# Performance work log

Measured on AMD Instinct MI355X. Metric: run time of the kernel, lower is better.

The kernel has to match this reference:

```python
import jax, jax.numpy as jnp
import numpy as np

B, T = 32, 512
DA, DV = 1280, 768
D = DA + DV          # fused audio+video feature dim = 2048
DM = 256             # mamba d_model
L = 4                # n_layers
DI = 2 * DM          # d_inner (expand=2)
DS = 16              # d_state
DC = 4               # d_conv
R = DM // 16         # dt_rank = ceil(256/16)
H = 128              # attn-pool hidden
NC = 8               # emotion classes
EPS_TIN = 1e-5
EPS_LN = 1e-5


def _ln(x, g, b):
    mu = x.mean(-1, keepdims=True)
    v = ((x - mu) ** 2).mean(-1, keepdims=True)
    return (x - mu) / jnp.sqrt(v + EPS_LN) * g + b


def _mamba(u, in_w, cw, cb, xw, dtw, dtb, A_log, Dp, ow):
    # u: [B,T,DM] -> [B,T,DM]; Mamba(v1) selective scan, d_state=16, d_conv=4, expand=2
    xz = jnp.einsum('btd,ed->bte', u, in_w)            # [B,T,2*DI]
    x, z = xz[..., :DI], xz[..., DI:]
    xp = jnp.pad(x, ((0, 0), (DC - 1, 0), (0, 0)))     # causal depthwise conv1d
    xc = sum(xp[:, k:k + u.shape[1], :] * cw[:, k] for k in range(DC)) + cb
    x = jax.nn.silu(xc)
    dbc = jnp.einsum('btd,ed->bte', x, xw)             # [B,T,R+2*DS]
    dt = jax.nn.softplus(jnp.einsum('btr,dr->btd', dbc[..., :R], dtw) + dtb)
    Bm = dbc[..., R:R + DS]
    Cm = dbc[..., R + DS:]
    A = -jnp.exp(A_log)                                # [DI,DS]

    def step(h, inp):
        dt_t, B_t, C_t, x_t = inp                      # [B,DI],[B,DS],[B,DS],[B,DI]
        h = jnp.exp(dt_t[..., None] * A) * h + dt_t[..., None] * B_t[:, None, :] * x_t[..., None]
        return h, jnp.einsum('bds,bs->bd', h, C_t)

    h0 = jnp.zeros((u.shape[0], DI, DS), u.dtype)
    xs = (dt.swapaxes(0, 1), Bm.swapaxes(0, 1), Cm.swapaxes(0, 1), x.swapaxes(0, 1))
    _, ys = jax.lax.scan(step, h0, xs)
    y = ys.swapaxes(0, 1) + Dp * x
    y = y * jax.nn.silu(z)
    return jnp.einsum('bti,oi->bto', y, ow)


def _forward(x, tin_gamma, tin_beta, proj_w, proj_b, ln_g, ln_b, in_proj_w, conv_w, conv_b,
             x_proj_w, dt_proj_w, dt_proj_b, A_log, D_param, out_proj_w,
             out_ln_g, out_ln_b, res_scale, attn_w1, attn_b1, attn_w2, head_w, head_b, lengths):
    mask = jnp.arange(T)[None, :] < lengths[:, None]   # [B,T]
    m = mask[..., None].astype(x.dtype)
    # FusedTIN: masked temporal instance norm + affine
    denom = jnp.maximum(lengths, 1).astype(x.dtype)[:, None, None]
    mean = (x * m).sum(1, keepdims=True) / denom
    var = (((x - mean) ** 2) * m).sum(1, keepdims=True) / denom
    xn = (x - mean) / jnp.sqrt(var + EPS_TIN) * m
    xn = (xn * tin_gamma + tin_beta) * m
    # MambaStack: proj_in + prenorm residual mamba blocks (dropout = eval identity)
    h = jnp.einsum('btd,md->btm', xn, proj_w) + proj_b
    for l in range(L):
        y = _mamba(_ln(h, ln_g[l], ln_b[l]), in_proj_w[l], conv_w[l], conv_b[l],
                   x_proj_w[l], dt_proj_w[l], dt_proj_b[l], A_log[l], D_param[l], out_proj_w[l])
        h = h + res_scale * y
    h = _ln(h, out_ln_g, out_ln_b)
    # MaskedAttnPool
    s = jnp.einsum('bth,oh->bto', jnp.tanh(jnp.einsum('btd,hd->bth', h, attn_w1) + attn_b1), attn_w2)[..., 0]
    logits = jnp.where(mask, s, -jnp.inf)
    alpha = jnp.nan_to_num(jax.nn.softmax(logits, axis=1)) * mask
    alpha = alpha / jnp.clip(alpha.sum(1, keepdims=True), 1e-9)
    ctx = (alpha[..., None] * h).sum(1)
    # classifier head
    return jnp.einsum('bd,cd->bc', ctx, head_w) + head_b


def setup_inputs() -> dict:
    key = jax.random.key(0)
    ks = jax.random.split(key, 16)
    s = 0.05
    inp = {}
    inp['x'] = jax.random.normal(ks[0], (B, T, D), jnp.float32)
    inp['lengths'] = jax.random.randint(ks[1], (B,), T // 4, T + 1)
    inp['tin_gamma'] = jnp.ones((D,), jnp.float32)
    inp['tin_beta'] = jnp.zeros((D,), jnp.float32)
    inp['proj_w'] = jax.random.normal(ks[2], (DM, D), jnp.float32) * s
    inp['proj_b'] = jnp.zeros((DM,), jnp.float32)
    inp['ln_g'] = jnp.ones((L, DM), jnp.float32)
    inp['ln_b'] = jnp.zeros((L, DM), jnp.float32)
    inp['in_proj_w'] = jax.random.normal(ks[3], (L, 2 * DI, DM), jnp.float32) * s
    inp['conv_w'] = jax.random.normal(ks[4], (L, DI, DC), jnp.float32) * s
    inp['conv_b'] = jnp.zeros((L, DI), jnp.float32)
    inp['x_proj_w'] = jax.random.normal(ks[5], (L, R + 2 * DS, DI), jnp.float32) * s
    inp['dt_proj_w'] = jax.random.normal(ks[6], (L, DI, R), jnp.float32) * s
    inp['dt_proj_b'] = jnp.full((L, DI), -3.0, jnp.float32) + jax.random.normal(ks[7], (L, DI), jnp.float32) * 0.1
    inp['A_log'] = jnp.log(jnp.broadcast_to(jnp.arange(1, DS + 1, dtype=jnp.float32), (L, DI, DS)) + 0.0)
    inp['D_param'] = jnp.ones((L, DI), jnp.float32)
    inp['out_proj_w'] = jax.random.normal(ks[8], (L, DM, DI), jnp.float32) * s
    inp['out_ln_g'] = jnp.ones((DM,), jnp.float32)
    inp['out_ln_b'] = jnp.zeros((DM,), jnp.float32)
    inp['res_scale'] = jnp.asarray(0.1, jnp.float32)
    inp['attn_w1'] = jax.random.normal(ks[9], (H, DM), jnp.float32) * s
    inp['attn_b1'] = jnp.zeros((H,), jnp.float32)
    inp['attn_w2'] = jax.random.normal(ks[10], (1, H), jnp.float32) * s
    inp['head_w'] = jax.random.normal(ks[11], (NC, DM), jnp.float32) * s
    inp['head_b'] = jnp.zeros((NC,), jnp.float32)
    return inp


def reference(x, tin_gamma, tin_beta, proj_w, proj_b, ln_g, ln_b, in_proj_w, conv_w, conv_b,
              x_proj_w, dt_proj_w, dt_proj_b, A_log, D_param, out_proj_w,
              out_ln_g, out_ln_b, res_scale, attn_w1, attn_b1, attn_w2, head_w, head_b, lengths):
    return _forward(x, tin_gamma, tin_beta, proj_w, proj_b, ln_g, ln_b, in_proj_w, conv_w, conv_b,
                    x_proj_w, dt_proj_w, dt_proj_b, A_log, D_param, out_proj_w,
                    out_ln_g, out_ln_b, res_scale, attn_w1, attn_b1, attn_w2, head_w, head_b, lengths)
```

## Files before the change

### kernel.cpp

```cpp
#include <hip/hip_runtime.h>

#define NB 32
#define NT 512
#define ND 2048
#define NDM 256
#define NDI 512
#define NDS 16
#define NR 16
#define NH 128
#define NNC 8
#define NL 4
#define NM (NB*NT)

typedef __attribute__((ext_vector_type(8))) short short8;
typedef __attribute__((ext_vector_type(4))) float floatx4;

__device__ __forceinline__ unsigned short f2bf_rn(float f) {
    unsigned u = __builtin_bit_cast(unsigned, f);
    u += 0x7FFFu + ((u >> 16) & 1u);
    return (unsigned short)(u >> 16);
}
__device__ __forceinline__ void cvt8(const float* v, short8& h8, short8& l8) {
#pragma unroll
    for (int q = 0; q < 8; ++q) {
        unsigned short hb = f2bf_rn(v[q]);
        float hf = __builtin_bit_cast(float, (unsigned)hb << 16);
        h8[q] = (short)hb;
        l8[q] = (short)f2bf_rn(v[q] - hf);
    }
}
__device__ __forceinline__ float quad_sum(float v) {
    int i = __builtin_bit_cast(int, v);
    int j = __builtin_amdgcn_update_dpp(0, i, 0xB1, 0xF, 0xF, true);
    v += __builtin_bit_cast(float, j);
    i = __builtin_bit_cast(int, v);
    j = __builtin_amdgcn_update_dpp(0, i, 0x4E, 0xF, 0xF, true);
    v += __builtin_bit_cast(float, j);
    return v;
}
__device__ __forceinline__ void glds16(const short* g, short* lds_base) {
    __builtin_amdgcn_global_load_lds(
        (const __attribute__((address_space(1))) void*)g,
        (__attribute__((address_space(3))) void*)lds_base, 16, 0, 0);
}

__global__ __launch_bounds__(256) void tin_stats_k(
    const float* __restrict__ x, const int* __restrict__ lengths,
    float* __restrict__ mean, float* __restrict__ rstd)
{
    __shared__ float rs_[4][64];
    __shared__ float rq_[4][64];
    const int b = blockIdx.x >> 5;
    const int d0 = (blockIdx.x & 31) << 6;
    const int dl = threadIdx.x & 63;
    const int strip = threadIdx.x >> 6;
    const int len = lengths[b];
    const int d = d0 + dl;
    float s = 0.f, q = 0.f;
    for (int t = strip; t < len; t += 4) {
        float v = x[((size_t)(b*NT + t))*ND + d];
        s += v; q += v*v;
    }
    rs_[strip][dl] = s; rq_[strip][dl] = q;
    __syncthreads();
    if (threadIdx.x < 64) {
        float S = rs_[0][dl]+rs_[1][dl]+rs_[2][dl]+rs_[3][dl];
        float Q = rq_[0][dl]+rq_[1][dl]+rq_[2][dl]+rq_[3][dl];
        float inv = 1.f / (float)(len < 1 ? 1 : len);
        float mu = S * inv;
        float var = Q * inv - mu*mu;
        mean[b*ND + d] = mu;
        rstd[b*ND + d] = rsqrtf(var + 1e-5f);
    }
}

#define SLN 264
__global__ __launch_bounds__(256) void tin_norm_k(
    const float* __restrict__ x, const int* __restrict__ lengths,
    const float* __restrict__ mean, const float* __restrict__ rstd,
    const float* __restrict__ g, const float* __restrict__ be,
    short* __restrict__ Oh, short* __restrict__ Ol)
{
    __shared__ float sT[16][SLN];
    const int tid = threadIdx.x;
    const int row = tid >> 4, c = tid & 15;
    const int m = blockIdx.x*16 + row;
    const int b = m >> 9, t = m & (NT-1);
    const int len = lengths[b];
    const int kg0 = blockIdx.y*256 + c*16;
    if (t >= len) {
#pragma unroll
        for (int i = 0; i < 16; ++i) sT[row][c*16 + i] = 0.f;
    } else {
#pragma unroll
        for (int qq = 0; qq < 4; ++qq) {
            const int kg = kg0 + qq*4;
            float4 v = *(const float4*)(x + (size_t)m*ND + kg);
            float4 mn = *(const float4*)(mean + b*ND + kg);
            float4 rr = *(const float4*)(rstd + b*ND + kg);
            float4 gg = *(const float4*)(g + kg);
            float4 bb = *(const float4*)(be + kg);
            sT[row][c*16+qq*4+0] = (v.x-mn.x)*rr.x*gg.x + bb.x;
            sT[row][c*16+qq*4+1] = (v.y-mn.y)*rr.y*gg.y + bb.y;
            sT[row][c*16+qq*4+2] = (v.z-mn.z)*rr.z*gg.z + bb.z;
            sT[row][c*16+qq*4+3] = (v.w-mn.w)*rr.w*gg.w + bb.w;
        }
    }
    __syncthreads();
#pragma unroll
    for (int q = 0; q < 2; ++q) {
        const int slot = tid + 256*q;
        const int tile = slot >> 6, ln2 = slot & 63;
        const int mr = ln2 & 15, kc = ln2 >> 4;
        float v[8];
        *(float4*)&v[0] = *(const float4*)&sT[mr][tile*32 + kc*8];
        *(float4*)&v[4] = *(const float4*)&sT[mr][tile*32 + kc*8 + 4];
        short8 h8, l8; cvt8(v, h8, l8);
        const size_t off = ((size_t)blockIdx.x*64 + blockIdx.y*8 + tile)*512 + ln2*8;
        *(short8*)(Oh + off) = h8;
        *(short8*)(Ol + off) = l8;
    }
}

__global__ __launch_bounds__(256) void wconv_k(
    const float* __restrict__ W, short* __restrict__ Oh, short* __restrict__ Ol,
    int K, int nmod, int nvalid)
{
    __shared__ float sT[16][SLN];
    const int tid = threadIdx.x;
    const int row = tid >> 4, c = tid & 15;
    const int n = blockIdx.x*16 + row;
    const int rr = n % nmod;
    const int kg0 = blockIdx.y*256 + c*16;
    if (rr >= nvalid) {
#pragma unroll
        for (int i = 0; i < 16; ++i) sT[row][c*16 + i] = 0.f;
    } else {
        const int src = (n/nmod)*nvalid + rr;
#pragma unroll
        for (int qq = 0; qq < 4; ++qq) {
            float4 v = *(const float4*)(W + (size_t)src*K + kg0 + qq*4);
            *(float4*)&sT[row][c*16+qq*4] = v;
        }
    }
    __syncthreads();
#pragma unroll
    for (int q = 0; q < 2; ++q) {
        const int slot = tid + 256*q;
        const int tile = slot >> 6, ln2 = slot & 63;
        const int mr = ln2 & 15, kc = ln2 >> 4;
        float v[8];
        *(float4*)&v[0] = *(const float4*)&sT[mr][tile*32 + kc*8];
        *(float4*)&v[4] = *(const float4*)&sT[mr][tile*32 + kc*8 + 4];
        short8 h8, l8; cvt8(v, h8, l8);
        const size_t off = ((size_t)blockIdx.x*(K>>5) + blockIdx.y*8 + tile)*512 + ln2*8;
        *(short8*)(Oh + off) = h8;
        *(short8*)(Ol + off) = l8;
    }
}

template<int MSUB, int NSUB, int EPI, int ATOMIC>
__global__ __launch_bounds__(256) void mgemm_k(
    const short* __restrict__ Ah, const short* __restrict__ Al,
    const short* __restrict__ Bh, const short* __restrict__ Bl,
    const float* __restrict__ bias, float* __restrict__ C,
    int ldc, int Nvalid, int K, const float* __restrict__ rsp)
{
    __shared__ __align__(16) short lds[(MSUB+NSUB)*1024];
    short* As_h = lds;
    short* As_l = lds + MSUB*512;
    short* Bs_h = lds + MSUB*1024;
    short* Bs_l = lds + MSUB*1024 + NSUB*512;
    const int tid = threadIdx.x, lane = tid & 63, w = tid >> 6;
    const int m0t = blockIdx.x * MSUB;
    const int n0t = blockIdx.y * NSUB;
    const int Ktiles = K >> 5;
    const int kslice = Ktiles / (int)gridDim.z;
    const int kt0 = blockIdx.z * kslice;
    constexpr int MI = MSUB/2, NI = NSUB/2;
    constexpr int ASG = MSUB/4, BSG = NSUB/4;
    const int wm = w >> 1, wn = w & 1;

    floatx4 acc[MI][NI] = {};

    for (int kk = 0; kk < kslice; ++kk) {
        const int kb = kt0 + kk;
#pragma unroll
        for (int u = 0; u < ASG; ++u) {
            const int sub = w*ASG + u;
            const size_t off = ((size_t)(m0t + sub)*Ktiles + kb)*512 + lane*8;
            glds16(Ah + off, &As_h[sub*512]);
            glds16(Al + off, &As_l[sub*512]);
        }
#pragma unroll
        for (int u = 0; u < BSG; ++u) {
            const int sub = w*BSG + u;
            const size_t off = ((size_t)(n0t + sub)*Ktiles + kb)*512 + lane*8;
            glds16(Bh + off, &Bs_h[sub*512]);
            glds16(Bl + off, &Bs_l[sub*512]);
        }
        __syncthreads();
        short8 fah[MI], fal[MI], fbh[NI], fbl[NI];
#pragma unroll
        for (int i = 0; i < MI; ++i) {
            const int sub = wm*MI + i;
            fah[i] = *(const short8*)&As_h[sub*512 + lane*8];
            fal[i] = *(const short8*)&As_l[sub*512 + lane*8];
        }
#pragma unroll
        for (int j = 0; j < NI; ++j) {
            const int sub = wn*NI + j;
            fbh[j] = *(const short8*)&Bs_h[sub*512 + lane*8];
            fbl[j] = *(const short8*)&Bs_l[sub*512 + lane*8];
        }
#pragma unroll
        for (int i = 0; i < MI; ++i)
#pragma unroll
            for (int j = 0; j < NI; ++j) {
                acc[i][j] = __builtin_amdgcn_mfma_f32_16x16x32_bf16(fah[i], fbh[j], acc[i][j], 0, 0, 0);
                acc[i][j] = __builtin_amdgcn_mfma_f32_16x16x32_bf16(fah[i], fbl[j], acc[i][j], 0, 0, 0);
                acc[i][j] = __builtin_amdgcn_mfma_f32_16x16x32_bf16(fal[i], fbh[j], acc[i][j], 0, 0, 0);
            }
        __syncthreads();
    }

    const float rs = (EPI == 1) ? rsp[0] : 0.f;
    const int lc = lane >> 4, col = lane & 15;
    const bool addb = (EPI != 1) && bias && (!ATOMIC || blockIdx.z == 0);
#pragma unroll
    for (int j = 0; j < NI; ++j) {
        const int n = (n0t + wn*NI + j)*16 + col;
        if (n < Nvalid) {
            const float bv = addb ? bias[n] : 0.f;
#pragma unroll
            for (int i = 0; i < MI; ++i) {
                const int mb = (m0t + wm*MI + i)*16 + lc*4;
#pragma unroll
                for (int r = 0; r < 4; ++r) {
                    float v = acc[i][j][r];
                    float* cp = C + (size_t)(mb + r)*ldc + n;
                    if (ATOMIC) {
                        if (EPI == 1) atomicAdd(cp, rs*v);
                        else          atomicAdd(cp, v + bv);
                    } else {
                        if (EPI == 0)      *cp = v + bv;
                        else if (EPI == 1) *cp = fmaf(rs, v, *cp);
                        else               *cp = tanhf(v + bv);
                    }
                }
            }
        }
    }
}

template<int WF32>
__global__ __launch_bounds__(256) void ln_blk_k(
    const float* __restrict__ in, const float* __restrict__ g,
    const float* __restrict__ b,
    short* __restrict__ Oh, short* __restrict__ Ol, float* __restrict__ o32)
{
    __shared__ float sT[16][SLN];
    const int tid = threadIdx.x;
    const int row = tid >> 4, c = tid & 15;
    const int m = blockIdx.x*16 + row;
    float v[16];
#pragma unroll
    for (int qq = 0; qq < 4; ++qq)
        *(float4*)&v[qq*4] = *(const float4*)(in + (size_t)m*NDM + c*16 + qq*4);
    float s = 0.f, q = 0.f;
#pragma unroll
    for (int i = 0; i < 16; ++i) { s += v[i]; q += v[i]*v[i]; }
#pragma unroll
    for (int o = 8; o; o >>= 1) { s += __shfl_xor(s, o); q += __shfl_xor(q, o); }
    const float mu = s * (1.f/NDM);
    const float r = rsqrtf(q*(1.f/NDM) - mu*mu + 1e-5f);
#pragma unroll
    for (int i = 0; i < 16; ++i) {
        const int kg = c*16 + i;
        v[i] = (v[i]-mu)*r*g[kg] + b[kg];
        sT[row][kg] = v[i];
    }
    if (WF32) {
#pragma unroll
        for (int qq = 0; qq < 4; ++qq)
            *(float4*)(o32 + (size_t)m*NDM + c*16 + qq*4) = *(const float4*)&v[qq*4];
    }
    __syncthreads();
#pragma unroll
    for (int qv = 0; qv < 2; ++qv) {
        const int slot = tid + 256*qv;
        const int tile = slot >> 6, ln2 = slot & 63;
        const int mr = ln2 & 15, kc = ln2 >> 4;
        float vv[8];
        *(float4*)&vv[0] = *(const float4*)&sT[mr][tile*32 + kc*8];
        *(float4*)&vv[4] = *(const float4*)&sT[mr][tile*32 + kc*8 + 4];
        short8 h8, l8; cvt8(vv, h8, l8);
        const size_t off = ((size_t)blockIdx.x*8 + tile)*512 + ln2*8;
        *(short8*)(Oh + off) = h8;
        *(short8*)(Ol + off) = l8;
    }
}

#define SCV 520
__global__ __launch_bounds__(256) void conv_blk_k(
    const float* __restrict__ xz, const float* __restrict__ cw,
    const float* __restrict__ cb, float* __restrict__ xc32,
    short* __restrict__ Oh, short* __restrict__ Ol)
{
    __shared__ float sT[16][SCV];
    const int tid = threadIdx.x;
    const int row = tid >> 4, cg = tid & 15;
    const int m = blockIdx.x*16 + row;
    const int t = m & (NT-1);
#pragma unroll
    for (int grp = 0; grp < 4; ++grp) {
        const int ch = cg*32 + grp*8;
        float a[8];
        *(float4*)&a[0] = *(const float4*)(cb + ch);
        *(float4*)&a[4] = *(const float4*)(cb + ch + 4);
        float4 wv[8];
#pragma unroll
        for (int i = 0; i < 8; ++i) wv[i] = *(const float4*)(cw + (ch+i)*4);
#pragma unroll
        for (int kk = 0; kk < 4; ++kk) {
            if (t - 3 + kk >= 0) {
                const float* xp = xz + (size_t)(m-3+kk)*(2*NDI) + ch;
                float xv[8];
                *(float4*)&xv[0] = *(const float4*)xp;
                *(float4*)&xv[4] = *(const float4*)(xp + 4);
                const float tap[8] = {
                    kk==0?wv[0].x:kk==1?wv[0].y:kk==2?wv[0].z:wv[0].w,
                    kk==0?wv[1].x:kk==1?wv[1].y:kk==2?wv[1].z:wv[1].w,
                    kk==0?wv[2].x:kk==1?wv[2].y:kk==2?wv[2].z:wv[2].w,
                    kk==0?wv[3].x:kk==1?wv[3].y:kk==2?wv[3].z:wv[3].w,
                    kk==0?wv[4].x:kk==1?wv[4].y:kk==2?wv[4].z:wv[4].w,
                    kk==0?wv[5].x:kk==1?wv[5].y:kk==2?wv[5].z:wv[5].w,
                    kk==0?wv[6].x:kk==1?wv[6].y:kk==2?wv[6].z:wv[6].w,
                    kk==0?wv[7].x:kk==1?wv[7].y:kk==2?wv[7].z:wv[7].w};
#pragma unroll
                for (int i = 0; i < 8; ++i) a[i] = fmaf(xv[i], tap[i], a[i]);
            }
        }
#pragma unroll
        for (int i = 0; i < 8; ++i) a[i] = a[i] / (1.f + __expf(-a[i]));
        *(float4*)&sT[row][ch] = *(const float4*)&a[0];
        *(float4*)&sT[row][ch+4] = *(const float4*)&a[4];
        *(float4*)(xc32 + (size_t)m*NDI + ch) = *(const float4*)&a[0];
        *(float4*)(xc32 + (size_t)m*NDI + ch + 4) = *(const float4*)&a[4];
    }
    __syncthreads();
#pragma unroll
    for (int q = 0; q < 4; ++q) {
        const int slot = tid + 256*q;
        const int tile = slot >> 6, ln2 = slot & 63;
        const int mr = ln2 & 15, kc = ln2 >> 4;
        float vv[8];
        *(float4*)&vv[0] = *(const float4*)&sT[mr][tile*32 + kc*8];
        *(float4*)&vv[4] = *(const float4*)&sT[mr][tile*32 + kc*8 + 4];
        short8 h8, l8; cvt8(vv, h8, l8);
        const size_t off = ((size_t)blockIdx.x*16 + tile)*512 + ln2*8;
        *(short8*)(Oh + off) = h8;
        *(short8*)(Ol + off) = l8;
    }
}

__global__ __launch_bounds__(256) void dt_k(
    const float* __restrict__ dbc, const float* __restrict__ dtw,
    const float* __restrict__ dtb, float* __restrict__ dt)
{
    const int m = blockIdx.x;
    const float* rsrc = dbc + (size_t)m*48;
    float rv[16];
#pragma unroll
    for (int i = 0; i < 16; ++i) rv[i] = rsrc[i];
#pragma unroll
    for (int hh = 0; hh < 2; ++hh) {
        const int d = hh*256 + threadIdx.x;
        const float* wr = dtw + d*16;
        float a = dtb[d];
#pragma unroll
        for (int i = 0; i < 16; ++i) a = fmaf(rv[i], wr[i], a);
        dt[(size_t)m*NDI + d] = (a > 20.f) ? a : log1pf(__expf(a));
    }
}

__global__ __launch_bounds__(256) void scan_k(
    const float* __restrict__ dbc, const float* __restrict__ dtp,
    const float* __restrict__ xcp, const float* __restrict__ xz,
    const float* __restrict__ Alog, const float* __restrict__ Dp,
    short* __restrict__ Yh, short* __restrict__ Yl)
{
    __shared__ float sBC[64][32];
    __shared__ float sDt[64][68];
    __shared__ float sX[64][68];
    __shared__ float sY[64][68];
    const int tid = threadIdx.x;
    const int w = tid >> 6, lane = tid & 63;
    const int dl = lane >> 2, sg = lane & 3;
    const int b = blockIdx.x >> 3;
    const int d0 = (blockIdx.x & 7) << 6;
    const int dloc = w*16 + dl;
    const int d = d0 + dloc;
    float ar[4];
    {
        float4 al4 = *(const float4*)(Alog + d*NDS + sg*4);
        ar[0] = -__expf(al4.x); ar[1] = -__expf(al4.y);
        ar[2] = -__expf(al4.z); ar[3] = -__expf(al4.w);
    }
    const float Dpv = Dp[d];
    float hr[4] = {0.f, 0.f, 0.f, 0.f};
    const int mbase = b*NT;
    const int srow = tid >> 2, sq = (tid & 3) << 3;
    const int tr = tid >> 2, qq = tid & 3;

    for (int c0 = 0; c0 < NT; c0 += 64) {
        __syncthreads();
        {
            const float* dp_ = dbc + (size_t)(mbase + c0 + srow)*48 + 16 + sq;
            *(float4*)&sBC[srow][sq]   = *(const float4*)dp_;
            *(float4*)&sBC[srow][sq+4] = *(const float4*)(dp_ + 4);
        }
        {
            const float* dsrc = dtp + (size_t)(mbase + c0 + tr)*NDI + d0 + qq*16;
            const float* xsrc = xcp + (size_t)(mbase + c0 + tr)*NDI + d0 + qq*16;
#pragma unroll
            for (int i = 0; i < 4; ++i) {
                float4 dv = *(const float4*)(dsrc + i*4);
                float4 xv = *(const float4*)(xsrc + i*4);
                const int dd = qq*16 + i*4;
                sDt[dd+0][tr]=dv.x; sDt[dd+1][tr]=dv.y; sDt[dd+2][tr]=dv.z; sDt[dd+3][tr]=dv.w;
                sX[dd+0][tr]=xv.x;  sX[dd+1][tr]=xv.y;  sX[dd+2][tr]=xv.z;  sX[dd+3][tr]=xv.w;
            }
        }
        __syncthreads();
        float4 Bt[2][4], Ct[2][4], dt4[2], x4[2];
#pragma unroll
        for (int i = 0; i < 4; ++i) {
            Bt[0][i] = *(const float4*)&sBC[i][sg*4];
            Ct[0][i] = *(const float4*)&sBC[i][16 + sg*4];
        }
        dt4[0] = *(const float4*)&sDt[dloc][0];
        x4[0]  = *(const float4*)&sX[dloc][0];
#pragma unroll
        for (int g = 0; g < 16; ++g) {
            const int cur = g & 1, nxt = cur ^ 1;
            if (g < 15) {
                const int t4 = (g+1)*4;
#pragma unroll
                for (int i = 0; i < 4; ++i) {
                    Bt[nxt][i] = *(const float4*)&sBC[t4+i][sg*4];
                    Ct[nxt][i] = *(const float4*)&sBC[t4+i][16 + sg*4];
                }
                dt4[nxt] = *(const float4*)&sDt[dloc][t4];
                x4[nxt]  = *(const float4*)&sX[dloc][t4];
            }
#pragma unroll
            for (int i = 0; i < 4; ++i) {
                const float dtv = (i==0)?dt4[cur].x:(i==1)?dt4[cur].y:(i==2)?dt4[cur].z:dt4[cur].w;
                const float xv  = (i==0)?x4[cur].x:(i==1)?x4[cur].y:(i==2)?x4[cur].z:x4[cur].w;
                const float4 Bv = Bt[cur][i];
                const float4 Cv = Ct[cur][i];
                const float dbx = dtv * xv;
                float pa0 = __expf(dtv*ar[0]);
                float pa1 = __expf(dtv*ar[1]);
                float pa2 = __expf(dtv*ar[2]);
                float pa3 = __expf(dtv*ar[3]);
                hr[0] = fmaf(pa0, hr[0], dbx*Bv.x);
                hr[1] = fmaf(pa1, hr[1], dbx*Bv.y);
                hr[2] = fmaf(pa2, hr[2], dbx*Bv.z);
                hr[3] = fmaf(pa3, hr[3], dbx*Bv.w);
                float cp = hr[0]*Cv.x;
                cp = fmaf(hr[1], Cv.y, cp);
                cp = fmaf(hr[2], Cv.z, cp);
                cp = fmaf(hr[3], Cv.w, cp);
                cp = quad_sum(cp);
                if (sg == 0) sY[g*4 + i][dloc] = fmaf(Dpv, xv, cp);
            }
        }
        __syncthreads();
#pragma unroll
        for (int q = 0; q < 2; ++q) {
            const int slot = tid + 256*q;
            const int tile = slot >> 6, ln2 = slot & 63;
            const int tm = tile >> 1, tk = tile & 1;
            const int mr = ln2 & 15, kc = ln2 >> 4;
            const int m = mbase + c0 + tm*16 + mr;
            const int kd = d0 + tk*32 + kc*8;
            float yv[8];
            *(float4*)&yv[0] = *(const float4*)&sY[tm*16 + mr][tk*32 + kc*8];
            *(float4*)&yv[4] = *(const float4*)&sY[tm*16 + mr][tk*32 + kc*8 + 4];
            float zv[8];
            *(float4*)&zv[0] = *(const float4*)(xz + (size_t)m*(2*NDI) + NDI + kd);
            *(float4*)&zv[4] = *(const float4*)(xz + (size_t)m*(2*NDI) + NDI + kd + 4);
#pragma unroll
            for (int i = 0; i < 8; ++i)
                yv[i] *= zv[i] / (1.f + __expf(-zv[i]));
            short8 h8, l8; cvt8(yv, h8, l8);
            const size_t off = ((size_t)(m>>4)*16 + (kd>>5))*512 + ln2*8;
            *(short8*)(Yh + off) = h8;
            *(short8*)(Yl + off) = l8;
        }
    }
}

__global__ __launch_bounds__(64) void score_k(
    const float* __restrict__ t1, const float* __restrict__ w2,
    float* __restrict__ sout)
{
    const int m = blockIdx.x;
    const int lane = threadIdx.x;
    float v = t1[(size_t)m*NH + lane]*w2[lane]
            + t1[(size_t)m*NH + 64 + lane]*w2[64 + lane];
#pragma unroll
    for (int o = 32; o; o >>= 1) v += __shfl_xor(v, o);
    if (lane == 0) sout[m] = v;
}

__global__ __launch_bounds__(256) void pool_k(
    const float* __restrict__ sbuf, const float* __restrict__ u,
    const int* __restrict__ lengths, float* __restrict__ ctx)
{
    __shared__ float al[NT];
    __shared__ float red[256];
    const int b = blockIdx.x;
    const int tid = threadIdx.x;
    const int len = lengths[b];
    float mx = -3.4e38f;
    for (int t = tid; t < len; t += 256) mx = fmaxf(mx, sbuf[b*NT + t]);
    red[tid] = mx; __syncthreads();
    for (int o = 128; o; o >>= 1) { if (tid < o) red[tid] = fmaxf(red[tid], red[tid+o]); __syncthreads(); }
    mx = red[0];
    __syncthreads();
    float sm = 0.f;
    for (int t = tid; t < len; t += 256) {
        float e = __expf(sbuf[b*NT + t] - mx);
        al[t] = e; sm += e;
    }
    red[tid] = sm; __syncthreads();
    for (int o = 128; o; o >>= 1) { if (tid < o) red[tid] += red[tid+o]; __syncthreads(); }
    const float rZ = 1.f / red[0];
    float acc = 0.f;
    const float* up = u + (size_t)b*NT*NDM + tid;
    for (int t = 0; t < len; ++t) acc = fmaf(al[t], up[(size_t)t*NDM], acc);
    ctx[b*NDM + tid] = acc * rZ;
}

__global__ __launch_bounds__(64) void head_k(
    const float* __restrict__ ctx, const float* __restrict__ hw,
    const float* __restrict__ hb, float* __restrict__ o)
{
    const int b = blockIdx.x;
    const int lane = threadIdx.x;
    const float4 c4 = *(const float4*)(ctx + b*NDM + lane*4);
#pragma unroll
    for (int c = 0; c < NNC; ++c) {
        const float4 w4 = *(const float4*)(hw + c*NDM + lane*4);
        float v = c4.x*w4.x + c4.y*w4.y + c4.z*w4.z + c4.w*w4.w;
#pragma unroll
        for (int off = 32; off; off >>= 1) v += __shfl_xor(v, off);
        if (lane == 0) o[b*NNC + c] = v + hb[c];
    }
}

extern "C" void kernel_launch(void* const* d_in, const int* in_sizes, int n_in,
                              void* d_out, int out_size, void* d_ws, size_t ws_size,
                              hipStream_t stream)
{
    (void)in_sizes; (void)n_in; (void)out_size; (void)ws_size;
    const float* x         = (const float*)d_in[0];
    const int*   lengths   = (const int*)  d_in[1];
    const float* tin_gamma = (const float*)d_in[2];
    const float* tin_beta  = (const float*)d_in[3];
    const float* proj_w    = (const float*)d_in[4];
    const float* proj_b    = (const float*)d_in[5];
    const float* ln_g      = (const float*)d_in[6];
    const float* ln_b      = (const float*)d_in[7];
    const float* in_proj_w = (const float*)d_in[8];
    const float* conv_w    = (const float*)d_in[9];
    const float* conv_b    = (const float*)d_in[10];
    const float* x_proj_w  = (const float*)d_in[11];
    const float* dt_proj_w = (const float*)d_in[12];
    const float* dt_proj_b = (const float*)d_in[13];
    const float* A_log     = (const float*)d_in[14];
    const float* D_param   = (const float*)d_in[15];
    const float* out_proj_w= (const float*)d_in[16];
    const float* out_ln_g  = (const float*)d_in[17];
    const float* out_ln_b  = (const float*)d_in[18];
    const float* res_scale = (const float*)d_in[19];
    const float* attn_w1   = (const float*)d_in[20];
    const float* attn_b1   = (const float*)d_in[21];
    const float* attn_w2   = (const float*)d_in[22];
    const float* head_w    = (const float*)d_in[23];
    const float* head_b    = (const float*)d_in[24];
    float* out = (float*)d_out;

    float* ws = (float*)d_ws;
    float* mean   = ws;
    float* rstd   = mean + 65536;
    float* hbuf   = rstd + 65536;
    float* ubuf32 = hbuf + (size_t)NM*NDM;
    float* dbc    = ubuf32 + (size_t)NM*NDM;
    float* t1     = dbc + (size_t)NM*48;
    float* sbuf   = t1 + (size_t)NM*NH;
    float* ctx    = sbuf + NM;
    float* fend   = ctx + NB*NDM;
    short* ublk_h = (short*)fend;
    short* ublk_l = ublk_h + (size_t)NM*NDM;
    short* xcb_h  = ublk_l + (size_t)NM*NDM;
    short* xcb_l  = xcb_h + (size_t)NM*NDI;
    short* yq_h   = xcb_l + (size_t)NM*NDI;
    short* yq_l   = yq_h + (size_t)NM*NDI;
    short* pw_h   = yq_l + (size_t)NM*NDI;
    short* pw_l   = pw_h + (size_t)256*2048;
    short* iw_h   = pw_l + (size_t)256*2048;
    short* iw_l   = iw_h + (size_t)4*1024*256;
    short* xw_h   = iw_l + (size_t)4*1024*256;
    short* xw_l   = xw_h + (size_t)4*64*512;
    short* ow_h   = xw_l + (size_t)4*64*512;
    short* ow_l   = ow_h + (size_t)4*256*512;
    short* aw_h   = ow_l + (size_t)4*256*512;
    short* aw_l   = aw_h + (size_t)128*256;
    float* over   = (float*)(aw_l + (size_t)128*256);
    short* xn_h   = (short*)over;
    short* xn_l   = xn_h + (size_t)NM*ND;
    float* xz     = over;
    float* xc32   = over + (size_t)NM*2*NDI;
    float* dtb_   = xc32 + (size_t)NM*NDI;

    const dim3 blk(256);

    wconv_k<<<dim3(16, 8), blk, 0, stream>>>(proj_w, pw_h, pw_l, 2048, 1<<28, 1<<28);
    wconv_k<<<dim3(256, 1), blk, 0, stream>>>(in_proj_w, iw_h, iw_l, 256, 1<<28, 1<<28);
    wconv_k<<<dim3(16, 2), blk, 0, stream>>>(x_proj_w, xw_h, xw_l, 512, 64, 48);
    wconv_k<<<dim3(64, 2), blk, 0, stream>>>(out_proj_w, ow_h, ow_l, 512, 1<<28, 1<<28);
    wconv_k<<<dim3(8, 1), blk, 0, stream>>>(attn_w1, aw_h, aw_l, 256, 1<<28, 1<<28);

    tin_stats_k<<<dim3(NB*32), blk, 0, stream>>>(x, lengths, mean, rstd);
    tin_norm_k<<<dim3(NM/16, 8), blk, 0, stream>>>(x, lengths, mean, rstd,
        tin_gamma, tin_beta, xn_h, xn_l);
    hipMemsetAsync(hbuf, 0, (size_t)NM*NDM*sizeof(float), stream);
    mgemm_k<4,8,0,1><<<dim3(256, 2, 4), blk, 0, stream>>>(
        xn_h, xn_l, pw_h, pw_l, proj_b, hbuf, NDM, NDM, 2048, nullptr);

    for (int l = 0; l < NL; ++l) {
        ln_blk_k<0><<<dim3(NM/16), blk, 0, stream>>>(
            hbuf, ln_g + l*NDM, ln_b + l*NDM, ublk_h, ublk_l, nullptr);
        mgemm_k<8,8,0,0><<<dim3(128, 8, 1), blk, 0, stream>>>(
            ublk_h, ublk_l, iw_h + (size_t)l*1024*256, iw_l + (size_t)l*1024*256,
            nullptr, xz, 2*NDI, 2*NDI, NDM, nullptr);
        conv_blk_k<<<dim3(NM/16), blk, 0, stream>>>(
            xz, conv_w + (size_t)l*NDI*4, conv_b + (size_t)l*NDI, xc32, xcb_h, xcb_l);
        hipMemsetAsync(dbc, 0, (size_t)NM*48*sizeof(float), stream);
        mgemm_k<4,4,0,1><<<dim3(256, 1, 2), blk, 0, stream>>>(
            xcb_h, xcb_l, xw_h + (size_t)l*64*512, xw_l + (size_t)l*64*512,
            nullptr, dbc, 48, 48, 512, nullptr);
        dt_k<<<dim3(NM), blk, 0, stream>>>(
            dbc, dt_proj_w + (size_t)l*NDI*NR, dt_proj_b + (size_t)l*NDI, dtb_);
        scan_k<<<dim3(NB*8), blk, 0, stream>>>(
            dbc, dtb_, xc32, xz, A_log + (size_t)l*NDI*NDS, D_param + (size_t)l*NDI,
            yq_h, yq_l);
        mgemm_k<4,8,1,1><<<dim3(256, 2, 2), blk, 0, stream>>>(
            yq_h, yq_l, ow_h + (size_t)l*256*512, ow_l + (size_t)l*256*512,
            nullptr, hbuf, NDM, NDM, 512, res_scale);
    }

    ln_blk_k<1><<<dim3(NM/16), blk, 0, stream>>>(
        hbuf, out_ln_g, out_ln_b, ublk_h, ublk_l, ubuf32);
    mgemm_k<4,4,2,0><<<dim3(256, 2, 1), blk, 0, stream>>>(
        ublk_h, ublk_l, aw_h, aw_l, attn_b1, t1, NH, NH, 256, nullptr);
    score_k<<<dim3(NM), dim3(64), 0, stream>>>(t1, attn_w2, sbuf);
    pool_k<<<dim3(NB), blk, 0, stream>>>(sbuf, ubuf32, lengths, ctx);
    head_k<<<dim3(NB), dim3(64), 0, stream>>>(ctx, head_w, head_b, out);
}
```

Measured before the change: 1.584 ms.

## Double-buffer GEMM LDS staging, drop split-K atomics, fuse dt projection into scan

The GEMM kernel now double-buffers its LDS tiles so the next K-tile's global-to-LDS copy is issued before the current tile's MFMAs, removing one barrier per iteration. Split-K with atomicAdd and its memsets is removed; each block now covers the full K range with plain stores, and the projection GEMM moves to 8x8 tiles. The separate dt_k kernel is fused into scan_k, which computes the softplus dt projection in LDS from the dbc rows, avoiding a large dt round trip through global memory. In exchange, the GEMMs launch fewer blocks with longer K loops, and the scan blocks take on the extra dt arithmetic.

```diff
diff --git a/kernel.cpp b/kernel.cpp
--- a/kernel.cpp
+++ b/kernel.cpp
@@ -159,32 +159,30 @@
     }
 }
 
-template<int MSUB, int NSUB, int EPI, int ATOMIC>
+template<int MSUB, int NSUB, int EPI>
 __global__ __launch_bounds__(256) void mgemm_k(
     const short* __restrict__ Ah, const short* __restrict__ Al,
     const short* __restrict__ Bh, const short* __restrict__ Bl,
     const float* __restrict__ bias, float* __restrict__ C,
     int ldc, int Nvalid, int K, const float* __restrict__ rsp)
 {
-    __shared__ __align__(16) short lds[(MSUB+NSUB)*1024];
-    short* As_h = lds;
-    short* As_l = lds + MSUB*512;
-    short* Bs_h = lds + MSUB*1024;
-    short* Bs_l = lds + MSUB*1024 + NSUB*512;
+    constexpr int STG = (MSUB+NSUB)*1024;
+    __shared__ __align__(16) short lds[2*STG];
     const int tid = threadIdx.x, lane = tid & 63, w = tid >> 6;
     const int m0t = blockIdx.x * MSUB;
     const int n0t = blockIdx.y * NSUB;
     const int Ktiles = K >> 5;
-    const int kslice = Ktiles / (int)gridDim.z;
-    const int kt0 = blockIdx.z * kslice;
     constexpr int MI = MSUB/2, NI = NSUB/2;
     constexpr int ASG = MSUB/4, BSG = NSUB/4;
     const int wm = w >> 1, wn = w & 1;
 
     floatx4 acc[MI][NI] = {};
 
-    for (int kk = 0; kk < kslice; ++kk) {
-        const int kb = kt0 + kk;
+    auto stage = [&](int kb, int buf) {
+        short* As_h = lds + buf*STG;
+        short* As_l = As_h + MSUB*512;
+        short* Bs_h = lds + buf*STG + MSUB*1024;
+        short* Bs_l = Bs_h + NSUB*512;
 #pragma unroll
         for (int u = 0; u < ASG; ++u) {
             const int sub = w*ASG + u;
@@ -199,7 +197,17 @@
             glds16(Bh + off, &Bs_h[sub*512]);
             glds16(Bl + off, &Bs_l[sub*512]);
         }
+    };
+
+    stage(0, 0);
+    for (int kb = 0; kb < Ktiles; ++kb) {
         __syncthreads();
+        if (kb + 1 < Ktiles) stage(kb + 1, (kb + 1) & 1);
+        const int buf = kb & 1;
+        const short* As_h = lds + buf*STG;
+        const short* As_l = As_h + MSUB*512;
+        const short* Bs_h = lds + buf*STG + MSUB*1024;
+        const short* Bs_l = Bs_h + NSUB*512;
         short8 fah[MI], fal[MI], fbh[NI], fbl[NI];
 #pragma unroll
         for (int i = 0; i < MI; ++i) {
@@ -221,17 +229,15 @@
                 acc[i][j] = __builtin_amdgcn_mfma_f32_16x16x32_bf16(fah[i], fbl[j], acc[i][j], 0, 0, 0);
                 acc[i][j] = __builtin_amdgcn_mfma_f32_16x16x32_bf16(fal[i], fbh[j], acc[i][j], 0, 0, 0);
             }
-        __syncthreads();
     }
 
     const float rs = (EPI == 1) ? rsp[0] : 0.f;
     const int lc = lane >> 4, col = lane & 15;
-    const bool addb = (EPI != 1) && bias && (!ATOMIC || blockIdx.z == 0);
 #pragma unroll
     for (int j = 0; j < NI; ++j) {
         const int n = (n0t + wn*NI + j)*16 + col;
         if (n < Nvalid) {
-            const float bv = addb ? bias[n] : 0.f;
+            const float bv = (EPI != 1 && bias) ? bias[n] : 0.f;
 #pragma unroll
             for (int i = 0; i < MI; ++i) {
                 const int mb = (m0t + wm*MI + i)*16 + lc*4;
@@ -239,14 +245,9 @@
                 for (int r = 0; r < 4; ++r) {
                     float v = acc[i][j][r];
                     float* cp = C + (size_t)(mb + r)*ldc + n;
-                    if (ATOMIC) {
-                        if (EPI == 1) atomicAdd(cp, rs*v);
-                        else          atomicAdd(cp, v + bv);
-                    } else {
-                        if (EPI == 0)      *cp = v + bv;
-                        else if (EPI == 1) *cp = fmaf(rs, v, *cp);
-                        else               *cp = tanhf(v + bv);
-                    }
+                    if (EPI == 0)      *cp = v + bv;
+                    else if (EPI == 1) *cp = fmaf(rs, v, *cp);
+                    else               *cp = tanhf(v + bv);
                 }
             }
         }
@@ -364,41 +365,22 @@
     }
 }
 
-__global__ __launch_bounds__(256) void dt_k(
-    const float* __restrict__ dbc, const float* __restrict__ dtw,
-    const float* __restrict__ dtb, float* __restrict__ dt)
-{
-    const int m = blockIdx.x;
-    const float* rsrc = dbc + (size_t)m*48;
-    float rv[16];
-#pragma unroll
-    for (int i = 0; i < 16; ++i) rv[i] = rsrc[i];
-#pragma unroll
-    for (int hh = 0; hh < 2; ++hh) {
-        const int d = hh*256 + threadIdx.x;
-        const float* wr = dtw + d*16;
-        float a = dtb[d];
-#pragma unroll
-        for (int i = 0; i < 16; ++i) a = fmaf(rv[i], wr[i], a);
-        dt[(size_t)m*NDI + d] = (a > 20.f) ? a : log1pf(__expf(a));
-    }
-}
-
 __global__ __launch_bounds__(256) void scan_k(
-    const float* __restrict__ dbc, const float* __restrict__ dtp,
-    const float* __restrict__ xcp, const float* __restrict__ xz,
+    const float* __restrict__ dbc, const float* __restrict__ xcp,
+    const float* __restrict__ xz,
+    const float* __restrict__ dtw, const float* __restrict__ dtb,
     const float* __restrict__ Alog, const float* __restrict__ Dp,
     short* __restrict__ Yh, short* __restrict__ Yl)
 {
-    __shared__ float sBC[64][32];
-    __shared__ float sDt[64][68];
+    __shared__ float sBC[64][52];
+    __shared__ float sDt[64][52];
     __shared__ float sX[64][68];
     __shared__ float sY[64][68];
     const int tid = threadIdx.x;
     const int w = tid >> 6, lane = tid & 63;
     const int dl = lane >> 2, sg = lane & 3;
     const int b = blockIdx.x >> 3;
-    const int d0 = (blockIdx.x & 7) << 6;
+    const int d0 = (blockIdx.x & 7) << 4 << 2;
     const int dloc = w*16 + dl;
     const int d = d0 + dloc;
     float ar[4];
@@ -408,39 +390,59 @@
         ar[2] = -__expf(al4.z); ar[3] = -__expf(al4.w);
     }
     const float Dpv = Dp[d];
+    const int dldt = lane;
+    float wr[16];
+#pragma unroll
+    for (int r4 = 0; r4 < 4; ++r4)
+        *(float4*)&wr[r4*4] = *(const float4*)(dtw + (size_t)(d0 + dldt)*NR + r4*4);
+    const float dtbv = dtb[d0 + dldt];
+
     float hr[4] = {0.f, 0.f, 0.f, 0.f};
     const int mbase = b*NT;
-    const int srow = tid >> 2, sq = (tid & 3) << 3;
-    const int tr = tid >> 2, qq = tid & 3;
 
     for (int c0 = 0; c0 < NT; c0 += 64) {
-        __syncthreads();
         {
-            const float* dp_ = dbc + (size_t)(mbase + c0 + srow)*48 + 16 + sq;
-            *(float4*)&sBC[srow][sq]   = *(const float4*)dp_;
-            *(float4*)&sBC[srow][sq+4] = *(const float4*)(dp_ + 4);
+            const int row = tid >> 2, q = tid & 3;
+            const float* dp_ = dbc + (size_t)(mbase + c0 + row)*48 + q*12;
+            *(float4*)&sBC[row][q*12]     = *(const float4*)dp_;
+            *(float4*)&sBC[row][q*12 + 4] = *(const float4*)(dp_ + 4);
+            *(float4*)&sBC[row][q*12 + 8] = *(const float4*)(dp_ + 8);
         }
         {
-            const float* dsrc = dtp + (size_t)(mbase + c0 + tr)*NDI + d0 + qq*16;
+            const int tr = tid >> 2, qq = tid & 3;
             const float* xsrc = xcp + (size_t)(mbase + c0 + tr)*NDI + d0 + qq*16;
 #pragma unroll
             for (int i = 0; i < 4; ++i) {
-                float4 dv = *(const float4*)(dsrc + i*4);
                 float4 xv = *(const float4*)(xsrc + i*4);
                 const int dd = qq*16 + i*4;
-                sDt[dd+0][tr]=dv.x; sDt[dd+1][tr]=dv.y; sDt[dd+2][tr]=dv.z; sDt[dd+3][tr]=dv.w;
-                sX[dd+0][tr]=xv.x;  sX[dd+1][tr]=xv.y;  sX[dd+2][tr]=xv.z;  sX[dd+3][tr]=xv.w;
+                sX[dd+0][tr]=xv.x; sX[dd+1][tr]=xv.y; sX[dd+2][tr]=xv.z; sX[dd+3][tr]=xv.w;
             }
         }
         __syncthreads();
-        float4 Bt[2][4], Ct[2][4], dt4[2], x4[2];
+#pragma unroll
+        for (int q = 0; q < 16; ++q) {
+            const int t = w + 4*q;
+            float a = dtbv;
+#pragma unroll
+            for (int r4 = 0; r4 < 4; ++r4) {
+                const float4 rv = *(const float4*)&sBC[t][r4*4];
+                a = fmaf(rv.x, wr[r4*4+0], a);
+                a = fmaf(rv.y, wr[r4*4+1], a);
+                a = fmaf(rv.z, wr[r4*4+2], a);
+                a = fmaf(rv.w, wr[r4*4+3], a);
+            }
+            sDt[t][dldt] = (a > 20.f) ? a : log1pf(__expf(a));
+        }
+        __syncthreads();
+        float4 Bt[2][4], Ct[2][4], x4[2];
+        float dts[2][4];
 #pragma unroll
         for (int i = 0; i < 4; ++i) {
-            Bt[0][i] = *(const float4*)&sBC[i][sg*4];
-            Ct[0][i] = *(const float4*)&sBC[i][16 + sg*4];
-        }
-        dt4[0] = *(const float4*)&sDt[dloc][0];
-        x4[0]  = *(const float4*)&sX[dloc][0];
+            Bt[0][i] = *(const float4*)&sBC[i][16 + sg*4];
+            Ct[0][i] = *(const float4*)&sBC[i][32 + sg*4];
+            dts[0][i] = sDt[i][dloc];
+        }
+        x4[0] = *(const float4*)&sX[dloc][0];
 #pragma unroll
         for (int g = 0; g < 16; ++g) {
             const int cur = g & 1, nxt = cur ^ 1;
@@ -448,15 +450,15 @@
                 const int t4 = (g+1)*4;
 #pragma unroll
                 for (int i = 0; i < 4; ++i) {
-                    Bt[nxt][i] = *(const float4*)&sBC[t4+i][sg*4];
-                    Ct[nxt][i] = *(const float4*)&sBC[t4+i][16 + sg*4];
+                    Bt[nxt][i] = *(const float4*)&sBC[t4+i][16 + sg*4];
+                    Ct[nxt][i] = *(const float4*)&sBC[t4+i][32 + sg*4];
+                    dts[nxt][i] = sDt[t4+i][dloc];
                 }
-                dt4[nxt] = *(const float4*)&sDt[dloc][t4];
-                x4[nxt]  = *(const float4*)&sX[dloc][t4];
+                x4[nxt] = *(const float4*)&sX[dloc][t4];
             }
 #pragma unroll
             for (int i = 0; i < 4; ++i) {
-                const float dtv = (i==0)?dt4[cur].x:(i==1)?dt4[cur].y:(i==2)?dt4[cur].z:dt4[cur].w;
+                const float dtv = dts[cur][i];
                 const float xv  = (i==0)?x4[cur].x:(i==1)?x4[cur].y:(i==2)?x4[cur].z:x4[cur].w;
                 const float4 Bv = Bt[cur][i];
                 const float4 Cv = Ct[cur][i];
@@ -500,6 +502,7 @@
             *(short8*)(Yh + off) = h8;
             *(short8*)(Yl + off) = l8;
         }
+        __syncthreads();
     }
 }
 
@@ -625,7 +628,6 @@
     short* xn_l   = xn_h + (size_t)NM*ND;
     float* xz     = over;
     float* xc32   = over + (size_t)NM*2*NDI;
-    float* dtb_   = xc32 + (size_t)NM*NDI;
 
     const dim3 blk(256);
 
@@ -638,35 +640,31 @@
     tin_stats_k<<<dim3(NB*32), blk, 0, stream>>>(x, lengths, mean, rstd);
     tin_norm_k<<<dim3(NM/16, 8), blk, 0, stream>>>(x, lengths, mean, rstd,
         tin_gamma, tin_beta, xn_h, xn_l);
-    hipMemsetAsync(hbuf, 0, (size_t)NM*NDM*sizeof(float), stream);
-    mgemm_k<4,8,0,1><<<dim3(256, 2, 4), blk, 0, stream>>>(
+    mgemm_k<8,8,0><<<dim3(NM/128, 2), blk, 0, stream>>>(
         xn_h, xn_l, pw_h, pw_l, proj_b, hbuf, NDM, NDM, 2048, nullptr);
 
     for (int l = 0; l < NL; ++l) {
         ln_blk_k<0><<<dim3(NM/16), blk, 0, stream>>>(
             hbuf, ln_g + l*NDM, ln_b + l*NDM, ublk_h, ublk_l, nullptr);
-        mgemm_k<8,8,0,0><<<dim3(128, 8, 1), blk, 0, stream>>>(
+        mgemm_k<4,8,0><<<dim3(NM/64, 8), blk, 0, stream>>>(
             ublk_h, ublk_l, iw_h + (size_t)l*1024*256, iw_l + (size_t)l*1024*256,
             nullptr, xz, 2*NDI, 2*NDI, NDM, nullptr);
         conv_blk_k<<<dim3(NM/16), blk, 0, stream>>>(
             xz, conv_w + (size_t)l*NDI*4, conv_b + (size_t)l*NDI, xc32, xcb_h, xcb_l);
-        hipMemsetAsync(dbc, 0, (size_t)NM*48*sizeof(float), stream);
-        mgemm_k<4,4,0,1><<<dim3(256, 1, 2), blk, 0, stream>>>(
+        mgemm_k<4,4,0><<<dim3(NM/64, 1), blk, 0, stream>>>(
             xcb_h, xcb_l, xw_h + (size_t)l*64*512, xw_l + (size_t)l*64*512,
             nullptr, dbc, 48, 48, 512, nullptr);
-        dt_k<<<dim3(NM), blk, 0, stream>>>(
-            dbc, dt_proj_w + (size_t)l*NDI*NR, dt_proj_b + (size_t)l*NDI, dtb_);
         scan_k<<<dim3(NB*8), blk, 0, stream>>>(
-            dbc, dtb_, xc32, xz, A_log + (size_t)l*NDI*NDS, D_param + (size_t)l*NDI,
-            yq_h, yq_l);
-        mgemm_k<4,8,1,1><<<dim3(256, 2, 2), blk, 0, stream>>>(
+            dbc, xc32, xz, dt_proj_w + (size_t)l*NDI*NR, dt_proj_b + (size_t)l*NDI,
+            A_log + (size_t)l*NDI*NDS, D_param + (size_t)l*NDI, yq_h, yq_l);
+        mgemm_k<4,8,1><<<dim3(NM/64, 2), blk, 0, stream>>>(
             yq_h, yq_l, ow_h + (size_t)l*256*512, ow_l + (size_t)l*256*512,
             nullptr, hbuf, NDM, NDM, 512, res_scale);
     }
 
     ln_blk_k<1><<<dim3(NM/16), blk, 0, stream>>>(
         hbuf, out_ln_g, out_ln_b, ublk_h, ublk_l, ubuf32);
-    mgemm_k<4,4,2,0><<<dim3(256, 2, 1), blk, 0, stream>>>(
+    mgemm_k<4,4,2><<<dim3(NM/64, 2), blk, 0, stream>>>(
         ublk_h, ublk_l, aw_h, aw_l, attn_b1, t1, NH, NH, 256, nullptr);
     score_k<<<dim3(NM), dim3(64), 0, stream>>>(t1, attn_w2, sbuf);
     pool_k<<<dim3(NB), blk, 0, stream>>>(sbuf, ubuf32, lengths, ctx);
```

Result: faster. 1.504 ms (-5.1%).
